# Optimization experiments

Hardware: AMD Instinct MI355X
Metric: run time of the kernel (lower is better)

## Reference

```python
import jax, jax.numpy as jnp
import numpy as np

B, T, D = 8, 4096, 1024
H, HD = 8, 128            # head_dim = ceil(D/H)
P = H * HD                # proj_dim = 1024
OUT = 1024
WIN, STRIDE = 64, 32


def _window_index(seq_len, win, stride):
    # mirrors the Python start-list construction in RollingAttentionPooling.forward
    starts = list(range(0, max(1, seq_len), stride))
    if starts and starts[-1] + win < seq_len:
        starts.append(seq_len - win)
    starts = sorted(set(max(0, s) for s in starts))
    idx = np.asarray(starts)[:, None] + np.arange(win)[None, :]
    valid = idx < seq_len
    idx = np.minimum(idx, seq_len - 1)
    return jnp.asarray(idx, dtype=jnp.int32), jnp.asarray(valid)


def setup_inputs() -> dict:
    key = jax.random.key(0)
    k0, k1, k2, k3 = jax.random.split(key, 4)
    x = jax.random.normal(k0, (B, T, D), dtype=jnp.float32)
    w_kv = jax.random.normal(k1, (D, 2 * P), dtype=jnp.float32) * 0.02
    query = jax.random.normal(k2, (H, HD), dtype=jnp.float32)
    w_out_w = jax.random.normal(k3, (OUT, P), dtype=jnp.float32) * 0.02
    w_out_b = jnp.zeros((OUT,), dtype=jnp.float32)
    return {"x": x, "w_kv": w_kv, "query": query, "w_out_w": w_out_w, "w_out_b": w_out_b}


def reference(x, w_kv, query, w_out_w, w_out_b):
    bsz, seq_len, _ = x.shape
    # K/V projection computed once for the whole sequence (same math as
    # recomputing per-window, since windows are slices of x).
    kv = (x @ w_kv).reshape(bsz, seq_len, 2, H, HD)
    k = kv[:, :, 0]                                   # (B, T, H, HD)
    v = kv[:, :, 1]                                   # (B, T, H, HD)
    logits = jnp.einsum('bthd,hd->bht', k, query) / jnp.sqrt(jnp.float32(HD))

    idx, valid = _window_index(seq_len, WIN, STRIDE)
    lw = logits[:, :, idx]
    lw = jnp.where(valid[None, None], lw, -jnp.inf)
    scores = jax.nn.softmax(lw.astype(jnp.float32), axis=-1).astype(v.dtype)
    vw = v[:, idx]
    pooled = jnp.einsum('bhwt,bwthd->bwhd', scores, vw)
    pooled = pooled.reshape(bsz, idx.shape[0], P)     # (B, W, P)
    out_w = pooled @ w_out_w.T + w_out_b              # (B, W, OUT)
    return out_w.mean(axis=1)                         # (B, OUT)
```

## Files before the change

### kernel.cpp

```cpp
#include <hip/hip_runtime.h>

#define B_ 8
#define T_ 4096
#define D_ 1024
#define H_ 8
#define HD_ 128
#define P_ 1024
#define OUT_ 1024
#define W_ 128
#define NC_ 64
#define CH_ 64
#define NPC_ 64
#define PCH_ 16

#define TRL_ 32

__global__ void __launch_bounds__(256) k_qproj(const float* __restrict__ w_kv,
                                               const float* __restrict__ query,
                                               float* __restrict__ qp) {
  int d = blockIdx.x;
  int t = threadIdx.x;
  float4 wv = ((const float4*)(w_kv + (size_t)d * (2 * P_)))[t];
  float4 qv = ((const float4*)query)[t];
  float a = wv.x * qv.x + wv.y * qv.y + wv.z * qv.z + wv.w * qv.w;
#pragma unroll
  for (int off = 16; off; off >>= 1) a += __shfl_xor(a, off, 64);
  if ((t & 31) == 0) {
    int h = t >> 5;
    qp[h * D_ + d] = a * 0.08838834764831845f;
  }
}

__global__ void __launch_bounds__(256, 4) k_logits(const float* __restrict__ x,
                                                   const float* __restrict__ qp,
                                                   float* __restrict__ logits) {
  __shared__ float s_q[H_ * D_];
  __shared__ float s_out[H_][TRL_ + 1];
  const int t = threadIdx.x;
  for (int i = t; i < H_ * D_ / 4; i += 256)
    ((float4*)s_q)[i] = ((const float4*)qp)[i];
  __syncthreads();

  const int w = t >> 6;
  const int l = t & 63;
  const int grp = l >> 4;
  const int c16 = l & 15;
  const int R0 = blockIdx.x * TRL_;
  const bool bb0 = (c16 & 1), bb1 = (c16 & 2), bb2 = (c16 & 4);
  const int hsel = (c16 & 1) * 4 + ((c16 >> 1) & 1) * 2 + ((c16 >> 2) & 1);

  const int lrow0 = w * 8 + grp * 2;
  const float4* xr0 = (const float4*)(x + ((size_t)(R0 + lrow0) << 10));
  const float4* xr1 = (const float4*)(x + ((size_t)(R0 + lrow0 + 1) << 10));

  float4 p40[H_], p41[H_];
#pragma unroll
  for (int h = 0; h < H_; ++h) {
    p40[h] = make_float4(0.f, 0.f, 0.f, 0.f);
    p41[h] = make_float4(0.f, 0.f, 0.f, 0.f);
  }

  auto fma8 = [&](const float4& xc0, const float4& xc1, int kc) {
    const float* qb = s_q + kc * 64 + c16 * 4;
#pragma unroll
    for (int h = 0; h < H_; ++h) {
      float4 qv = *(const float4*)(qb + h * D_);
      p40[h].x += xc0.x * qv.x; p40[h].y += xc0.y * qv.y;
      p40[h].z += xc0.z * qv.z; p40[h].w += xc0.w * qv.w;
      p41[h].x += xc1.x * qv.x; p41[h].y += xc1.y * qv.y;
      p41[h].z += xc1.z * qv.z; p41[h].w += xc1.w * qv.w;
    }
  };

  float4 a0 = xr0[0 * 16 + c16], a1 = xr1[0 * 16 + c16];
  float4 b0 = xr0[1 * 16 + c16], b1 = xr1[1 * 16 + c16];
  float4 c0 = xr0[2 * 16 + c16], c1 = xr1[2 * 16 + c16];
  float4 d0 = xr0[3 * 16 + c16], d1 = xr1[3 * 16 + c16];
#pragma unroll 1
  for (int kc4 = 0; kc4 < 3; ++kc4) {
    const int kc = kc4 * 4;
    fma8(a0, a1, kc);
    a0 = xr0[(kc + 4) * 16 + c16]; a1 = xr1[(kc + 4) * 16 + c16];
    fma8(b0, b1, kc + 1);
    b0 = xr0[(kc + 5) * 16 + c16]; b1 = xr1[(kc + 5) * 16 + c16];
    fma8(c0, c1, kc + 2);
    c0 = xr0[(kc + 6) * 16 + c16]; c1 = xr1[(kc + 6) * 16 + c16];
    fma8(d0, d1, kc + 3);
    d0 = xr0[(kc + 7) * 16 + c16]; d1 = xr1[(kc + 7) * 16 + c16];
  }
  fma8(a0, a1, 12);
  fma8(b0, b1, 13);
  fma8(c0, c1, 14);
  fma8(d0, d1, 15);

#pragma unroll
  for (int r = 0; r < 2; ++r) {
    float p[H_];
#pragma unroll
    for (int h = 0; h < H_; ++h) {
      float4 q = r ? p41[h] : p40[h];
      p[h] = (q.x + q.y) + (q.z + q.w);
    }
    float v0 = (bb0 ? p[4] : p[0]) + __shfl_xor(bb0 ? p[0] : p[4], 1, 64);
    float v1 = (bb0 ? p[5] : p[1]) + __shfl_xor(bb0 ? p[1] : p[5], 1, 64);
    float v2 = (bb0 ? p[6] : p[2]) + __shfl_xor(bb0 ? p[2] : p[6], 1, 64);
    float v3 = (bb0 ? p[7] : p[3]) + __shfl_xor(bb0 ? p[3] : p[7], 1, 64);
    float w0 = (bb1 ? v2 : v0) + __shfl_xor(bb1 ? v0 : v2, 2, 64);
    float w1 = (bb1 ? v3 : v1) + __shfl_xor(bb1 ? v1 : v3, 2, 64);
    float u = (bb2 ? w1 : w0) + __shfl_xor(bb2 ? w0 : w1, 4, 64);
    u += __shfl_xor(u, 8, 64);
    if (c16 < 8) s_out[hsel][lrow0 + r] = u;
  }
  __syncthreads();
  {
    int hh = t >> 5, j = t & 31;
    int b = R0 >> 12, t0 = R0 & (T_ - 1);
    logits[(((size_t)(b * H_ + hh)) << 12) + t0 + j] = s_out[hh][j];
  }
}

__global__ void __launch_bounds__(256) k_yacc(const float* __restrict__ x,
                                              const float* __restrict__ logits,
                                              float* __restrict__ partial) {
  int c = blockIdx.x;
  int b = blockIdx.y;
  int t0 = c * CH_;
  int W0 = (t0 >> 5) - 1;
  __shared__ float sw[CH_][H_];
  __shared__ float sm[4][H_], srs[4][H_];
  int tid = threadIdx.x;
  if (tid < 3 * H_) {
    int wi = tid >> 3, h = tid & 7;
    int w = W0 + wi;
    if (w >= 0 && w < W_) {
      const float* L = logits + (((size_t)(b * H_ + h)) << 12) + (w << 5);
      int cnt = min(64, T_ - (w << 5));
      float m = -1e30f;
#pragma unroll 8
      for (int i = 0; i < cnt; ++i) m = fmaxf(m, L[i]);
      float s = 0.f;
#pragma unroll 8
      for (int i = 0; i < cnt; ++i) s += __expf(L[i] - m);
      sm[wi][h] = m;
      srs[wi][h] = 1.0f / s;
    }
  }
  __syncthreads();
  const float invW = 1.0f / (float)W_;
  for (int i = tid; i < H_ * CH_; i += 256) {
    int h = i >> 6, tt = i & 63;
    int tg = t0 + tt;
    float l = logits[(((size_t)(b * H_ + h)) << 12) + tg];
    int w1 = tg >> 5;
    int rel = w1 - W0;
    float acc = __expf(l - sm[rel][h]) * srs[rel][h];
    if (w1 > 0) acc += __expf(l - sm[rel - 1][h]) * srs[rel - 1][h];
    sw[tt][h] = acc * invW;
  }
  __syncthreads();
  float4 acc[H_];
#pragma unroll
  for (int h = 0; h < H_; ++h) acc[h] = make_float4(0.f, 0.f, 0.f, 0.f);
  const float4* xb = (const float4*)(x + ((size_t)b * T_ + t0) * D_);
  for (int tt0 = 0; tt0 < CH_; tt0 += 8) {
    float4 xv[8];
#pragma unroll
    for (int j = 0; j < 8; ++j) xv[j] = xb[(tt0 + j) * (D_ / 4) + tid];
#pragma unroll
    for (int j = 0; j < 8; ++j) {
      float4 wa = *(const float4*)&sw[tt0 + j][0];
      float4 wb = *(const float4*)&sw[tt0 + j][4];
      acc[0].x += wa.x * xv[j].x; acc[0].y += wa.x * xv[j].y; acc[0].z += wa.x * xv[j].z; acc[0].w += wa.x * xv[j].w;
      acc[1].x += wa.y * xv[j].x; acc[1].y += wa.y * xv[j].y; acc[1].z += wa.y * xv[j].z; acc[1].w += wa.y * xv[j].w;
      acc[2].x += wa.z * xv[j].x; acc[2].y += wa.z * xv[j].y; acc[2].z += wa.z * xv[j].z; acc[2].w += wa.z * xv[j].w;
      acc[3].x += wa.w * xv[j].x; acc[3].y += wa.w * xv[j].y; acc[3].z += wa.w * xv[j].z; acc[3].w += wa.w * xv[j].w;
      acc[4].x += wb.x * xv[j].x; acc[4].y += wb.x * xv[j].y; acc[4].z += wb.x * xv[j].z; acc[4].w += wb.x * xv[j].w;
      acc[5].x += wb.y * xv[j].x; acc[5].y += wb.y * xv[j].y; acc[5].z += wb.y * xv[j].z; acc[5].w += wb.y * xv[j].w;
      acc[6].x += wb.z * xv[j].x; acc[6].y += wb.z * xv[j].y; acc[6].z += wb.z * xv[j].z; acc[6].w += wb.z * xv[j].w;
      acc[7].x += wb.w * xv[j].x; acc[7].y += wb.w * xv[j].y; acc[7].z += wb.w * xv[j].z; acc[7].w += wb.w * xv[j].w;
    }
  }
  float4* pp = (float4*)(partial + (((size_t)(c * B_ + b) * H_) << 10));
#pragma unroll
  for (int h = 0; h < H_; ++h) pp[h * (D_ / 4) + tid] = acc[h];
}

__global__ void __launch_bounds__(256) k_reduce_y(const float* __restrict__ partial,
                                                  float* __restrict__ y) {
  int i = blockIdx.x * blockDim.x + threadIdx.x;
  float4 a = make_float4(0.f, 0.f, 0.f, 0.f);
  const float4* p = (const float4*)partial;
#pragma unroll 8
  for (int c = 0; c < NC_; ++c) {
    float4 v = p[(size_t)c * (B_ * H_ * D_ / 4) + i];
    a.x += v.x; a.y += v.y; a.z += v.z; a.w += v.w;
  }
  ((float4*)y)[i] = a;
}

__global__ void __launch_bounds__(256) k_pooled_part(const float* __restrict__ y,
                                                     const float* __restrict__ w_kv,
                                                     float* __restrict__ ppart) {
  int c = blockIdx.x;
  int d0 = c * PCH_;
  int t = threadIdx.x;
  int h = t >> 5;
  __shared__ float sy[PCH_][B_ * H_];
  for (int i = t; i < PCH_ * B_ * H_; i += 256) {
    int dd = i >> 6, bh = i & 63;
    sy[dd][bh] = y[((size_t)bh << 10) + d0 + dd];
  }
  __syncthreads();
  float4 acc[B_];
#pragma unroll
  for (int b = 0; b < B_; ++b) acc[b] = make_float4(0.f, 0.f, 0.f, 0.f);
#pragma unroll
  for (int dd = 0; dd < PCH_; ++dd) {
    float4 wv = ((const float4*)(w_kv + (size_t)(d0 + dd) * (2 * P_) + P_))[t];
#pragma unroll
    for (int b = 0; b < B_; ++b) {
      float yv = sy[dd][b * H_ + h];
      acc[b].x += yv * wv.x; acc[b].y += yv * wv.y;
      acc[b].z += yv * wv.z; acc[b].w += yv * wv.w;
    }
  }
#pragma unroll
  for (int b = 0; b < B_; ++b)
    ((float4*)(ppart + (((size_t)c * B_ + b) << 10)))[t] = acc[b];
}

__global__ void __launch_bounds__(256) k_reduce_pooled(const float* __restrict__ ppart,
                                                       float* __restrict__ pooled) {
  int i = blockIdx.x * 256 + threadIdx.x;
  int b = i >> 8, p4 = i & 255;
  float4 a = make_float4(0.f, 0.f, 0.f, 0.f);
  const float4* p = (const float4*)ppart;
#pragma unroll 8
  for (int c = 0; c < NPC_; ++c) {
    float4 v = p[((c * B_ + b) << 8) + p4];
    a.x += v.x; a.y += v.y; a.z += v.z; a.w += v.w;
  }
  ((float4*)pooled)[i] = a;
}

__global__ void __launch_bounds__(256) k_out(const float* __restrict__ pooled,
                                             const float* __restrict__ w_out_w,
                                             const float* __restrict__ w_out_b,
                                             float* __restrict__ out) {
  int wid = threadIdx.x >> 6, lane = threadIdx.x & 63;
  int o = blockIdx.x * 4 + wid;
  const float4* wr = (const float4*)(w_out_w + (size_t)o * P_);
  float4 wv[4];
#pragma unroll
  for (int j = 0; j < 4; ++j) wv[j] = wr[lane + 64 * j];
  float res[B_];
#pragma unroll
  for (int b = 0; b < B_; ++b) {
    const float4* pb = (const float4*)(pooled + b * P_);
    float a = 0.f;
#pragma unroll
    for (int j = 0; j < 4; ++j) {
      float4 pv = pb[lane + 64 * j];
      a += wv[j].x * pv.x + wv[j].y * pv.y + wv[j].z * pv.z + wv[j].w * pv.w;
    }
#pragma unroll
    for (int off = 32; off; off >>= 1) a += __shfl_down(a, off, 64);
    res[b] = a;
  }
  if (lane == 0) {
    float bias = w_out_b[o];
#pragma unroll
    for (int b = 0; b < B_; ++b) out[b * OUT_ + o] = res[b] + bias;
  }
}

extern "C" void kernel_launch(void* const* d_in, const int* in_sizes, int n_in,
                              void* d_out, int out_size, void* d_ws, size_t ws_size,
                              hipStream_t stream) {
  const float* x       = (const float*)d_in[0];
  const float* w_kv    = (const float*)d_in[1];
  const float* query   = (const float*)d_in[2];
  const float* w_out_w = (const float*)d_in[3];
  const float* w_out_b = (const float*)d_in[4];
  float* out = (float*)d_out;

  float* ws = (float*)d_ws;
  float* qp      = ws;
  float* logits  = qp + H_ * D_;
  float* partial = logits + B_ * H_ * T_;
  float* y       = partial + (size_t)NC_ * B_ * H_ * D_;
  float* pooled  = y + B_ * H_ * D_;
  float* ppart   = partial;

  k_qproj<<<D_, 256, 0, stream>>>(w_kv, query, qp);
  k_logits<<<B_ * T_ / TRL_, 256, 0, stream>>>(x, qp, logits);
  k_yacc<<<dim3(NC_, B_), 256, 0, stream>>>(x, logits, partial);
  k_reduce_y<<<(B_ * H_ * D_ / 4) / 256, 256, 0, stream>>>(partial, y);
  k_pooled_part<<<NPC_, 256, 0, stream>>>(y, w_kv, ppart);
  k_reduce_pooled<<<(B_ * P_ / 4) / 256, 256, 0, stream>>>(ppart, pooled);
  k_out<<<OUT_ / 4, 256, 0, stream>>>(pooled, w_out_w, w_out_b, out);
}
```

Measured before the change: 308.6 us.

## Split logits kernel over D halves into two partial buffers summed in yacc

The logits kernel now splits the D=1024 reduction into two halves handled by separate blocks, doubling the grid and halving the shared-memory query tile (32KB to 16KB) so more blocks fit per CU. Each half writes its partial logits to its own buffer, and k_yacc sums the two buffers when it reads them. The accumulators also shrink from float4 to float2 chains using fmaf. The cost is an extra logits buffer, extra reads in k_yacc, and a different floating-point summation order.

```diff
diff --git a/kernel.cpp b/kernel.cpp
--- a/kernel.cpp
+++ b/kernel.cpp
@@ -31,75 +31,77 @@
   }
 }
 
-__global__ void __launch_bounds__(256, 4) k_logits(const float* __restrict__ x,
-                                                   const float* __restrict__ qp,
-                                                   float* __restrict__ logits) {
-  __shared__ float s_q[H_ * D_];
+__global__ void __launch_bounds__(256) k_logits(const float* __restrict__ x,
+                                                const float* __restrict__ qp,
+                                                float* __restrict__ lA,
+                                                float* __restrict__ lB) {
+  __shared__ float s_q[H_ * (D_ / 2)];
   __shared__ float s_out[H_][TRL_ + 1];
   const int t = threadIdx.x;
-  for (int i = t; i < H_ * D_ / 4; i += 256)
-    ((float4*)s_q)[i] = ((const float4*)qp)[i];
-  __syncthreads();
-
-  const int w = t >> 6;
-  const int l = t & 63;
+  const int half = blockIdx.x & 1;
+  const int rt = blockIdx.x >> 1;
+  {
+    const float4* qp4 = (const float4*)qp;
+#pragma unroll
+    for (int q = 0; q < 4; ++q) {
+      int i = t + 256 * q;
+      int h = i >> 7, j4 = i & 127;
+      ((float4*)s_q)[i] = qp4[h * 256 + half * 128 + j4];
+    }
+  }
+  __syncthreads();
+
+  const int w = t >> 6, l = t & 63;
   const int grp = l >> 4;
   const int c16 = l & 15;
-  const int R0 = blockIdx.x * TRL_;
+  const int R0 = rt * TRL_;
   const bool bb0 = (c16 & 1), bb1 = (c16 & 2), bb2 = (c16 & 4);
   const int hsel = (c16 & 1) * 4 + ((c16 >> 1) & 1) * 2 + ((c16 >> 2) & 1);
-
   const int lrow0 = w * 8 + grp * 2;
-  const float4* xr0 = (const float4*)(x + ((size_t)(R0 + lrow0) << 10));
-  const float4* xr1 = (const float4*)(x + ((size_t)(R0 + lrow0 + 1) << 10));
-
-  float4 p40[H_], p41[H_];
+
+  const float4* xr0 = (const float4*)x + (R0 + lrow0) * 256 + half * 128;
+  const float4* xr1 = xr0 + 256;
+
+  float2 p20[H_], p21[H_];
 #pragma unroll
   for (int h = 0; h < H_; ++h) {
-    p40[h] = make_float4(0.f, 0.f, 0.f, 0.f);
-    p41[h] = make_float4(0.f, 0.f, 0.f, 0.f);
-  }
-
-  auto fma8 = [&](const float4& xc0, const float4& xc1, int kc) {
-    const float* qb = s_q + kc * 64 + c16 * 4;
+    p20[h] = make_float2(0.f, 0.f);
+    p21[h] = make_float2(0.f, 0.f);
+  }
+
+  auto fma8 = [&](const float4 xc0, const float4 xc1, int kk) {
+    const float* qb = s_q + kk * 64 + c16 * 4;
 #pragma unroll
     for (int h = 0; h < H_; ++h) {
-      float4 qv = *(const float4*)(qb + h * D_);
-      p40[h].x += xc0.x * qv.x; p40[h].y += xc0.y * qv.y;
-      p40[h].z += xc0.z * qv.z; p40[h].w += xc0.w * qv.w;
-      p41[h].x += xc1.x * qv.x; p41[h].y += xc1.y * qv.y;
-      p41[h].z += xc1.z * qv.z; p41[h].w += xc1.w * qv.w;
+      float4 qv = *(const float4*)(qb + h * (D_ / 2));
+      p20[h].x = fmaf(xc0.x, qv.x, p20[h].x); p20[h].x = fmaf(xc0.z, qv.z, p20[h].x);
+      p20[h].y = fmaf(xc0.y, qv.y, p20[h].y); p20[h].y = fmaf(xc0.w, qv.w, p20[h].y);
+      p21[h].x = fmaf(xc1.x, qv.x, p21[h].x); p21[h].x = fmaf(xc1.z, qv.z, p21[h].x);
+      p21[h].y = fmaf(xc1.y, qv.y, p21[h].y); p21[h].y = fmaf(xc1.w, qv.w, p21[h].y);
     }
   };
 
-  float4 a0 = xr0[0 * 16 + c16], a1 = xr1[0 * 16 + c16];
-  float4 b0 = xr0[1 * 16 + c16], b1 = xr1[1 * 16 + c16];
-  float4 c0 = xr0[2 * 16 + c16], c1 = xr1[2 * 16 + c16];
-  float4 d0 = xr0[3 * 16 + c16], d1 = xr1[3 * 16 + c16];
+  float4 A0 = xr0[c16],      A1 = xr1[c16];
+  float4 B0 = xr0[16 + c16], B1 = xr1[16 + c16];
 #pragma unroll 1
-  for (int kc4 = 0; kc4 < 3; ++kc4) {
-    const int kc = kc4 * 4;
-    fma8(a0, a1, kc);
-    a0 = xr0[(kc + 4) * 16 + c16]; a1 = xr1[(kc + 4) * 16 + c16];
-    fma8(b0, b1, kc + 1);
-    b0 = xr0[(kc + 5) * 16 + c16]; b1 = xr1[(kc + 5) * 16 + c16];
-    fma8(c0, c1, kc + 2);
-    c0 = xr0[(kc + 6) * 16 + c16]; c1 = xr1[(kc + 6) * 16 + c16];
-    fma8(d0, d1, kc + 3);
-    d0 = xr0[(kc + 7) * 16 + c16]; d1 = xr1[(kc + 7) * 16 + c16];
-  }
-  fma8(a0, a1, 12);
-  fma8(b0, b1, 13);
-  fma8(c0, c1, 14);
-  fma8(d0, d1, 15);
+  for (int j = 0; j < 3; ++j) {
+    float4 tA0 = A0, tA1 = A1;
+    A0 = xr0[(2 * j + 2) * 16 + c16]; A1 = xr1[(2 * j + 2) * 16 + c16];
+    fma8(tA0, tA1, 2 * j);
+    float4 tB0 = B0, tB1 = B1;
+    B0 = xr0[(2 * j + 3) * 16 + c16]; B1 = xr1[(2 * j + 3) * 16 + c16];
+    fma8(tB0, tB1, 2 * j + 1);
+  }
+  fma8(A0, A1, 6);
+  fma8(B0, B1, 7);
 
 #pragma unroll
   for (int r = 0; r < 2; ++r) {
     float p[H_];
 #pragma unroll
     for (int h = 0; h < H_; ++h) {
-      float4 q = r ? p41[h] : p40[h];
-      p[h] = (q.x + q.y) + (q.z + q.w);
+      float2 q = r ? p21[h] : p20[h];
+      p[h] = q.x + q.y;
     }
     float v0 = (bb0 ? p[4] : p[0]) + __shfl_xor(bb0 ? p[0] : p[4], 1, 64);
     float v1 = (bb0 ? p[5] : p[1]) + __shfl_xor(bb0 ? p[1] : p[5], 1, 64);
@@ -113,14 +115,16 @@
   }
   __syncthreads();
   {
+    float* out = half ? lB : lA;
     int hh = t >> 5, j = t & 31;
     int b = R0 >> 12, t0 = R0 & (T_ - 1);
-    logits[(((size_t)(b * H_ + hh)) << 12) + t0 + j] = s_out[hh][j];
+    out[(((size_t)(b * H_ + hh)) << 12) + t0 + j] = s_out[hh][j];
   }
 }
 
 __global__ void __launch_bounds__(256) k_yacc(const float* __restrict__ x,
-                                              const float* __restrict__ logits,
+                                              const float* __restrict__ lA,
+                                              const float* __restrict__ lB,
                                               float* __restrict__ partial) {
   int c = blockIdx.x;
   int b = blockIdx.y;
@@ -133,14 +137,16 @@
     int wi = tid >> 3, h = tid & 7;
     int w = W0 + wi;
     if (w >= 0 && w < W_) {
-      const float* L = logits + (((size_t)(b * H_ + h)) << 12) + (w << 5);
+      size_t base = (((size_t)(b * H_ + h)) << 12) + (w << 5);
+      const float* LAp = lA + base;
+      const float* LBp = lB + base;
       int cnt = min(64, T_ - (w << 5));
       float m = -1e30f;
 #pragma unroll 8
-      for (int i = 0; i < cnt; ++i) m = fmaxf(m, L[i]);
+      for (int i = 0; i < cnt; ++i) m = fmaxf(m, LAp[i] + LBp[i]);
       float s = 0.f;
 #pragma unroll 8
-      for (int i = 0; i < cnt; ++i) s += __expf(L[i] - m);
+      for (int i = 0; i < cnt; ++i) s += __expf(LAp[i] + LBp[i] - m);
       sm[wi][h] = m;
       srs[wi][h] = 1.0f / s;
     }
@@ -150,7 +156,8 @@
   for (int i = tid; i < H_ * CH_; i += 256) {
     int h = i >> 6, tt = i & 63;
     int tg = t0 + tt;
-    float l = logits[(((size_t)(b * H_ + h)) << 12) + tg];
+    size_t idx = (((size_t)(b * H_ + h)) << 12) + tg;
+    float l = lA[idx] + lB[idx];
     int w1 = tg >> 5;
     int rel = w1 - W0;
     float acc = __expf(l - sm[rel][h]) * srs[rel][h];
@@ -286,15 +293,16 @@
 
   float* ws = (float*)d_ws;
   float* qp      = ws;
-  float* logits  = qp + H_ * D_;
-  float* partial = logits + B_ * H_ * T_;
+  float* lA      = qp + H_ * D_;
+  float* lB      = lA + B_ * H_ * T_;
+  float* partial = lB + B_ * H_ * T_;
   float* y       = partial + (size_t)NC_ * B_ * H_ * D_;
   float* pooled  = y + B_ * H_ * D_;
   float* ppart   = partial;
 
   k_qproj<<<D_, 256, 0, stream>>>(w_kv, query, qp);
-  k_logits<<<B_ * T_ / TRL_, 256, 0, stream>>>(x, qp, logits);
-  k_yacc<<<dim3(NC_, B_), 256, 0, stream>>>(x, logits, partial);
+  k_logits<<<2 * (B_ * T_ / TRL_), 256, 0, stream>>>(x, qp, lA, lB);
+  k_yacc<<<dim3(NC_, B_), 256, 0, stream>>>(x, lA, lB, partial);
   k_reduce_y<<<(B_ * H_ * D_ / 4) / 256, 256, 0, stream>>>(partial, y);
   k_pooled_part<<<NPC_, 256, 0, stream>>>(y, w_kv, ppart);
   k_reduce_pooled<<<(B_ * P_ / 4) / 256, 256, 0, stream>>>(ppart, pooled);
```

New measurement: 250.0 us. -19.0%, faster.
